# Optimization experiments

Hardware: AMD Instinct MI355X
Metric: run time of the kernel (lower is better)

The kernel has to match this reference:

```python
import jax, jax.numpy as jnp
import numpy as np

BN_EPS = 1e-5

def setup_inputs() -> dict:
    key = jax.random.key(0)
    ks = jax.random.split(key, 8)
    B, Cin, H, W = 4, 256, 64, 64
    Cqk, Cout = 128, 256
    x = jax.random.normal(ks[0], (B, Cin, H, W), dtype=jnp.float32)
    # 1x1 convs == per-pixel linear maps: weight [out, in], bias [out]
    Wq = jax.random.normal(ks[1], (Cqk, Cin), dtype=jnp.float32) * 0.05
    bq = jax.random.normal(ks[2], (Cqk,), dtype=jnp.float32) * 0.05
    Wk = jax.random.normal(ks[3], (Cqk, Cin), dtype=jnp.float32) * 0.05
    bk = jax.random.normal(ks[4], (Cqk,), dtype=jnp.float32) * 0.05
    Wv = jax.random.normal(ks[5], (Cout, Cin), dtype=jnp.float32) * 0.05
    bv = jax.random.normal(ks[6], (Cout,), dtype=jnp.float32) * 0.05
    gamma = jnp.ones((Cout,), dtype=jnp.float32)
    beta = jnp.zeros((Cout,), dtype=jnp.float32)
    return {"x": x, "Wq": Wq, "bq": bq, "Wk": Wk, "bk": bk,
            "Wv": Wv, "bv": bv, "gamma": gamma, "beta": beta}

def reference(x, Wq, bq, Wk, bk, Wv, bv, gamma, beta):
    B, Cin, H, W = x.shape
    N = H * W
    # 1x1 convs (per-pixel linear projections)
    q = jnp.einsum('bchw,oc->bohw', x, Wq) + bq[None, :, None, None]  # [B,Cqk,H,W]
    k = jnp.einsum('bchw,oc->bohw', x, Wk) + bk[None, :, None, None]  # [B,Cqk,H,W]
    v = jnp.einsum('bchw,oc->bohw', x, Wv) + bv[None, :, None, None]  # [B,Cout,H,W]
    # num_levels=1: bilinear interpolate to the same size is identity.
    qf = q.reshape(B, -1, N)   # [B,Cqk,N]
    kf = k.reshape(B, -1, N)   # [B,Cqk,N]
    vf = v.reshape(B, -1, N)   # [B,Cout,N]
    # score = q^T k, softmax over keys (no 1/sqrt(d) scaling, as in source)
    score = jnp.einsum('bcn,bcm->bnm', qf, kf)        # [B,N,N]
    att = jax.nn.softmax(score, axis=2)               # [B,N,N]
    w = jnp.einsum('bnm,bcm->bcn', att, vf)           # [B,Cout,N]
    merged = w.reshape(B, -1, H, W)                   # [B,Cout,H,W]
    # BatchNorm2d in training mode: batch stats over (B,H,W), biased variance
    mean = jnp.mean(merged, axis=(0, 2, 3), keepdims=True)
    var = jnp.var(merged, axis=(0, 2, 3), keepdims=True)
    norm = (merged - mean) * jax.lax.rsqrt(var + BN_EPS)
    return norm * gamma[None, :, None, None] + beta[None, :, None, None]
```

## Files before the change

### kernel.cpp

```cpp
#include <hip/hip_runtime.h>
#include <hip/hip_bf16.h>

typedef __attribute__((ext_vector_type(8))) _Float16 hfrag;
typedef __attribute__((ext_vector_type(4))) float ffrag;
typedef __attribute__((ext_vector_type(8))) unsigned short us8;
typedef __attribute__((ext_vector_type(4))) unsigned short us4;

#define DEVINL static __device__ __forceinline__
#define MFMAH(a, b, c)  __builtin_amdgcn_mfma_f32_16x16x32_f16((a), (b), (c), 0, 0, 0)

DEVINL void gload_lds16(const _Float16* g, _Float16* l) {
    __builtin_amdgcn_global_load_lds(
        (const __attribute__((address_space(1))) unsigned int*)g,
        (__attribute__((address_space(3))) unsigned int*)l, 16, 0, 0);
}

DEVINL int pkh(float a, float b) {
    typedef __attribute__((ext_vector_type(2))) __fp16 fp16x2;
    fp16x2 t = __builtin_amdgcn_cvt_pkrtz(a, b);
    union { fp16x2 h; int i; } u; u.h = t; return u.i;
}

DEVINL int permV(int p) {
    return (p & 35) | ((p & 8) << 1) | ((p & 4) << 1) | ((p & 16) >> 2);
}

__global__ void kprep(const float* __restrict__ Wq, const float* __restrict__ Wk,
                      const float* __restrict__ Wv, const float* __restrict__ bq,
                      const float* __restrict__ bk, const float* __restrict__ bv,
                      _Float16* __restrict__ Wh, float* __restrict__ ball) {
    int t = blockIdx.x * 256 + threadIdx.x;
    int o = t >> 8, c = t & 255;
    float v = (o < 128) ? Wq[o * 256 + c]
            : (o < 256) ? Wk[(o - 128) * 256 + c]
                        : Wv[(o - 256) * 256 + c];
    Wh[t] = (_Float16)v;
    if (c == 0) {
        ball[o] = (o < 128) ? bq[o] : (o < 256) ? bk[o - 128] : bv[o - 256];
    }
}

__global__ __launch_bounds__(256) void kproj(const float* __restrict__ x,
                                             const _Float16* __restrict__ Wh,
                                             const float* __restrict__ ball,
                                             _Float16* __restrict__ Qb,
                                             _Float16* __restrict__ Kb,
                                             _Float16* __restrict__ Vb) {
    __shared__ _Float16 sX[64 * 256];
    const int t = threadIdx.x;
    const int lane = t & 63;
    const int wv = t >> 6;
    const int l16 = lane & 15;
    const int lg = lane >> 4;
    const int b = blockIdx.x >> 6;
    const int n0 = (blockIdx.x & 63) << 6;
    const float* xb = x + (size_t)b * 256 * 4096 + n0;

    const int p = lane;
#pragma unroll
    for (int ci = 0; ci < 8; ++ci) {
        const int c0 = ci * 32 + (wv << 3);
        __align__(16) _Float16 th[8];
#pragma unroll
        for (int j = 0; j < 8; ++j) th[j] = (_Float16)xb[(size_t)(c0 + j) * 4096 + p];
        *(us8*)&sX[p * 256 + (c0 ^ ((p & 7) << 3))] = *(const us8*)th;
    }
    __syncthreads();

    ffrag accQK[16];
    ffrag accV[16];
#pragma unroll
    for (int i = 0; i < 16; ++i) {
        accQK[i] = ffrag{0.f, 0.f, 0.f, 0.f};
        accV[i]  = ffrag{0.f, 0.f, 0.f, 0.f};
    }
    const int rowx = 16 * wv + l16;
#pragma unroll
    for (int step = 0; step < 8; ++step) {
        const int cb = step * 32 + (lg << 3);
        hfrag ax = *(const hfrag*)&sX[rowx * 256 + (cb ^ ((rowx & 7) << 3))];
#pragma unroll
        for (int ct = 0; ct < 16; ++ct) {
            const int o = ct * 16 + l16;
            hfrag bw = *(const hfrag*)&Wh[o * 256 + cb];
            accQK[ct] = MFMAH(ax, bw, accQK[ct]);
        }
        hfrag bx[4];
#pragma unroll
        for (int c2 = 0; c2 < 4; ++c2) {
            const int px = c2 * 16 + l16;
            bx[c2] = *(const hfrag*)&sX[px * 256 + (cb ^ ((px & 7) << 3))];
        }
#pragma unroll
        for (int mt = 0; mt < 4; ++mt) {
            const int o = 256 + 64 * wv + 16 * mt + l16;
            hfrag aw = *(const hfrag*)&Wh[o * 256 + cb];
#pragma unroll
            for (int c2 = 0; c2 < 4; ++c2)
                accV[mt * 4 + c2] = MFMAH(aw, bx[c2], accV[mt * 4 + c2]);
        }
    }

#pragma unroll
    for (int ct = 0; ct < 16; ++ct) {
        const int o = ct * 16 + l16;
        const float bias = ball[o];
        _Float16* dst = (o < 128) ? Qb : Kb;
        const int oo = o & 127;
#pragma unroll
        for (int r = 0; r < 4; ++r) {
            const int px = 16 * wv + (lg << 2) + r;
            dst[((size_t)b * 4096 + n0 + px) * 128 + oo] = (_Float16)(accQK[ct][r] + bias);
        }
    }
#pragma unroll
    for (int mt = 0; mt < 4; ++mt) {
#pragma unroll
        for (int r = 0; r < 4; ++r) {
            const int o = 64 * wv + 16 * mt + (lg << 2) + r;
            const float bias = ball[256 + o];
#pragma unroll
            for (int c2 = 0; c2 < 4; ++c2) {
                const int px = c2 * 16 + l16;
                Vb[((size_t)b * 256 + o) * 4096 + n0 + permV(px)] =
                    (_Float16)(accV[mt * 4 + c2][r] + bias);
            }
        }
    }
}

__global__ __launch_bounds__(512, 4) void kattn(const _Float16* __restrict__ Qb,
                                                const _Float16* __restrict__ Kb,
                                                const _Float16* __restrict__ Vb,
                                                _Float16* __restrict__ pO,
                                                float* __restrict__ pML) {
    __shared__ __align__(16) _Float16 smem[24832];
    _Float16* sK = smem;
    _Float16* sV = smem + 8192;
    float* sml = (float*)(smem + 24576);

    const int t = threadIdx.x;
    const int lane = t & 63;
    const int wv = t >> 6;
    const int qg = wv & 3;
    const int kh = wv >> 2;
    const int l16 = lane & 15;
    const int lg = lane >> 4;

    const int blk = blockIdx.x;
    const int x8 = blk & 7;
    const int b = x8 >> 1;
    const int ksel = x8 & 1;
    const int qt4 = blk >> 3;
    const int n0 = qt4 << 6;
    const int kb = ksel << 11;

    const _Float16* Kg = Kb + (size_t)b * 4096 * 128;
    const _Float16* Vg = Vb + (size_t)b * 256 * 4096;

    hfrag aq[4];
    {
        const size_t gq = ((size_t)b * 4096 + n0 + 16 * qg + l16) * 128;
#pragma unroll
        for (int st = 0; st < 4; ++st)
            aq[st] = *(const hfrag*)&Qb[gq + st * 32 + lg * 8];
    }

    float m_ = -3e38f, l_ = 0.f;
    ffrag O[16];
#pragma unroll
    for (int i = 0; i < 16; ++i) O[i] = ffrag{0.f, 0.f, 0.f, 0.f};

    const int krow_in = lane >> 4;
    const int kcol = lane & 15;
    const int vrow_in = lane >> 3;
    const int vcol = lane & 7;

    for (int it = 0; it < 32; ++it) {
        const int k0 = kb + (it << 6);
        __builtin_amdgcn_s_barrier();
        __builtin_amdgcn_sched_barrier(0);
#pragma unroll
        for (int j = 0; j < 2; ++j) {
            const int c = 2 * wv + j;
            const int row = 4 * c + krow_in;
            gload_lds16(Kg + (size_t)(k0 + row) * 128 + ((kcol ^ (row & 7)) << 3),
                        sK + c * 512);
        }
        __builtin_amdgcn_sched_barrier(0);
#pragma unroll
        for (int j = 0; j < 4; ++j) {
            const int cv = 4 * wv + j;
            const int co = 8 * cv + vrow_in;
            gload_lds16(Vg + (size_t)co * 4096 + k0 + ((vcol ^ (co & 7)) << 3),
                        sV + cv * 512);
        }
        asm volatile("s_waitcnt vmcnt(4)" ::: "memory");
        __builtin_amdgcn_s_barrier();
        __builtin_amdgcn_sched_barrier(0);

        ffrag S[2];
        S[0] = ffrag{0.f, 0.f, 0.f, 0.f};
        S[1] = ffrag{0.f, 0.f, 0.f, 0.f};
#pragma unroll
        for (int kt = 0; kt < 2; ++kt) {
            const int rowk = kh * 32 + kt * 16 + l16;
            const int swz = (rowk & 7) << 3;
#pragma unroll
            for (int st = 0; st < 4; ++st) {
                hfrag ak = *(const hfrag*)&sK[rowk * 128 + ((st * 32 + lg * 8) ^ swz)];
                S[kt] = MFMAH(ak, aq[st], S[kt]);
            }
        }

        float mx = fmaxf(fmaxf(fmaxf(S[0][0], S[0][1]), fmaxf(S[0][2], S[0][3])),
                         fmaxf(fmaxf(S[1][0], S[1][1]), fmaxf(S[1][2], S[1][3])));
        mx = fmaxf(mx, __shfl_xor(mx, 16));
        mx = fmaxf(mx, __shfl_xor(mx, 32));
        if (__any(mx > m_ + 8.f)) {
            const float newm = fmaxf(m_, mx);
            const float sc = __expf(m_ - newm);
            m_ = newm;
            l_ *= sc;
#pragma unroll
            for (int i = 0; i < 16; ++i)
#pragma unroll
                for (int r = 0; r < 4; ++r) O[i][r] *= sc;
        }
        float e0[4], e1[4];
        float rs = 0.f;
#pragma unroll
        for (int r = 0; r < 4; ++r) {
            e0[r] = __expf(S[0][r] - m_);
            e1[r] = __expf(S[1][r] - m_);
            rs += e0[r] + e1[r];
        }
        rs += __shfl_xor(rs, 16);
        rs += __shfl_xor(rs, 32);
        l_ += rs;

        hfrag pb;
        {
            union { int i[4]; hfrag h; } u;
            u.i[0] = pkh(e0[0], e0[1]);
            u.i[1] = pkh(e0[2], e0[3]);
            u.i[2] = pkh(e1[0], e1[1]);
            u.i[3] = pkh(e1[2], e1[3]);
            pb = u.h;
        }

        asm volatile("s_waitcnt vmcnt(0)" ::: "memory");
        __builtin_amdgcn_s_barrier();
        __builtin_amdgcn_sched_barrier(0);

#pragma unroll
        for (int ct = 0; ct < 16; ++ct) {
            const int co = ct * 16 + l16;
            hfrag av = *(const hfrag*)&sV[co * 64 + ((kh * 32 + lg * 8) ^ ((co & 7) << 3))];
            O[ct] = MFMAH(av, pb, O[ct]);
        }
    }

    __syncthreads();
    _Float16* sE = smem;
    const int row = qg * 16 + l16;
    const int rsw = (row & 7) << 3;
    if (kh == 1) {
        const float invl = 1.f / l_;
#pragma unroll
        for (int ct = 0; ct < 16; ++ct)
#pragma unroll
            for (int r = 0; r < 4; ++r) {
                const int col = ct * 16 + lg * 4 + r;
                sE[row * 256 + (col ^ rsw)] = (_Float16)(O[ct][r] * invl);
            }
        if (lg == 0) ((float2*)sml)[row] = make_float2(m_, l_);
    }
    __syncthreads();
    const size_t mlbase = (size_t)(ksel * 4 + b) * 4096 + n0;
    if (kh == 0) {
        const float2 pml = ((const float2*)sml)[row];
        const float M = fmaxf(m_, pml.x);
        const float a = __expf(m_ - M), c = __expf(pml.x - M);
        const float newl = a * l_ + c * pml.y;
        const float wa = a / newl, wb = c * pml.y / newl;
        if (lg == 0) ((float2*)pML)[mlbase + row] = make_float2(M, newl);
#pragma unroll
        for (int ct = 0; ct < 16; ++ct)
#pragma unroll
            for (int r = 0; r < 4; ++r) {
                const int col = ct * 16 + lg * 4 + r;
                const int idx = row * 256 + (col ^ rsw);
                const float o1n = (float)sE[idx];
                sE[idx] = (_Float16)(wa * O[ct][r] + wb * o1n);
            }
    }
    __syncthreads();
    const size_t obase = ((size_t)(ksel * 4 + b) * 4096 + n0) * 256;
#pragma unroll
    for (int i = 0; i < 4; ++i) {
        const int idx = i * 512 + t;
        const int px = idx >> 5;
        const int cg = idx & 31;
        *(us8*)&pO[obase + (size_t)px * 256 + cg * 8] =
            *(const us8*)&sE[px * 256 + (cg ^ (px & 7)) * 8];
    }
}

__global__ __launch_bounds__(256) void kmerge(const _Float16* __restrict__ pO,
                                              const float* __restrict__ pML,
                                              _Float16* __restrict__ wbuf,
                                              float* __restrict__ part) {
    __shared__ float sacc[2048];
    __shared__ float sacc2[2048];
    const int t = threadIdx.x;
    const int rowloc = t >> 5;
    const int co8 = (t & 31) * 8;
    float s[8], s2[8];
#pragma unroll
    for (int j = 0; j < 8; ++j) { s[j] = 0.f; s2[j] = 0.f; }
#pragma unroll 2
    for (int i = 0; i < 8; ++i) {
        const int g = blockIdx.x * 64 + i * 8 + rowloc;
        const float2 ml0 = ((const float2*)pML)[g];
        const float2 ml1 = ((const float2*)pML)[16384 + g];
        const float M = fmaxf(ml0.x, ml1.x);
        const float a = __expf(ml0.x - M) * ml0.y;
        const float c = __expf(ml1.x - M) * ml1.y;
        const float inv = 1.f / (a + c);
        const float wa = a * inv, wc = c * inv;
        hfrag o0 = *(const hfrag*)&pO[(size_t)g * 256 + co8];
        hfrag o1 = *(const hfrag*)&pO[(size_t)(16384 + g) * 256 + co8];
        hfrag w;
#pragma unroll
        for (int j = 0; j < 8; ++j) {
            const float v = wa * (float)o0[j] + wc * (float)o1[j];
            w[j] = (_Float16)v;
            s[j] += v;
            s2[j] += v * v;
        }
        *(hfrag*)&wbuf[(size_t)g * 256 + co8] = w;
    }
#pragma unroll
    for (int j = 0; j < 8; ++j) {
        sacc[rowloc * 256 + co8 + j] = s[j];
        sacc2[rowloc * 256 + co8 + j] = s2[j];
    }
    __syncthreads();
    float p = 0.f, p2 = 0.f;
#pragma unroll
    for (int rl = 0; rl < 8; ++rl) {
        p  += sacc[rl * 256 + t];
        p2 += sacc2[rl * 256 + t];
    }
    part[blockIdx.x * 512 + t] = p;
    part[blockIdx.x * 512 + 256 + t] = p2;
}

__global__ void kstats2(const float* __restrict__ partial, float* __restrict__ stats) {
    const int ch = blockIdx.x;
    const int j = threadIdx.x;
    float s = 0.f;
#pragma unroll
    for (int i = 0; i < 4; ++i)
        s += partial[(size_t)(j + 64 * i) * 512 + ch];
    s += __shfl_xor(s, 1);
    s += __shfl_xor(s, 2);
    s += __shfl_xor(s, 4);
    s += __shfl_xor(s, 8);
    s += __shfl_xor(s, 16);
    s += __shfl_xor(s, 32);
    if (j == 0) stats[ch] = s;
}

__global__ __launch_bounds__(256) void kapply(const _Float16* __restrict__ w,
                                              const float* __restrict__ stats,
                                              const float* __restrict__ gamma,
                                              const float* __restrict__ beta,
                                              float* __restrict__ out) {
    __shared__ _Float16 sw[64 * 260];
    __shared__ float sscale[256];
    __shared__ float sshift[256];
    const int t = threadIdx.x;
    const int b = blockIdx.x >> 6;
    const int n0 = (blockIdx.x & 63) << 6;
    const _Float16* wb = w + ((size_t)b * 4096 + n0) * 256;
#pragma unroll
    for (int i = 0; i < 16; ++i) {
        const int chunk = i * 256 + t;
        const int p = chunk >> 6;
        const int cq = chunk & 63;
        *(us4*)&sw[p * 260 + cq * 4] = *(const us4*)&wb[p * 256 + cq * 4];
    }
    {
        const float mean = stats[t] * (1.f / 16384.f);
        const float var = stats[256 + t] * (1.f / 16384.f) - mean * mean;
        const float inv = rsqrtf(var + 1e-5f);
        const float sc = gamma[t] * inv;
        sscale[t] = sc;
        sshift[t] = beta[t] - mean * sc;
    }
    __syncthreads();
    const int p = t & 63;
    const int cg = t >> 6;
    float* ob = out + (size_t)b * 256 * 4096 + n0;
#pragma unroll 4
    for (int i = 0; i < 64; ++i) {
        const int co = i * 4 + cg;
        const float v = (float)sw[p * 260 + co];
        ob[(size_t)co * 4096 + p] = v * sscale[co] + sshift[co];
    }
}

extern "C" void kernel_launch(void* const* d_in, const int* in_sizes, int n_in,
                              void* d_out, int out_size, void* d_ws, size_t ws_size,
                              hipStream_t stream) {
    const float* x     = (const float*)d_in[0];
    const float* Wq    = (const float*)d_in[1];
    const float* bq    = (const float*)d_in[2];
    const float* Wk    = (const float*)d_in[3];
    const float* bk    = (const float*)d_in[4];
    const float* Wv    = (const float*)d_in[5];
    const float* bv    = (const float*)d_in[6];
    const float* gamma = (const float*)d_in[7];
    const float* beta  = (const float*)d_in[8];
    float* out = (float*)d_out;

    char* ws = (char*)d_ws;
    _Float16* Wh    = (_Float16*)(ws + 0x0);
    float*    pML   = (float*)(ws + 0x0);
    float*    ball  = (float*)(ws + 0x40000);
    float*    stats = (float*)(ws + 0x40800);
    float*    part  = (float*)(ws + 0x41000);
    _Float16* Qb    = (_Float16*)(ws + 0x100000);
    _Float16* Kb    = (_Float16*)(ws + 0x500000);
    _Float16* wbuf  = (_Float16*)(ws + 0x100000);
    _Float16* Vb    = (_Float16*)(ws + 0x900000);
    _Float16* pO    = (_Float16*)(ws + 0x1100000);
    if (ws_size < 0x2100000) return;

    kprep<<<512, 256, 0, stream>>>(Wq, Wk, Wv, bq, bk, bv, Wh, ball);
    kproj<<<256, 256, 0, stream>>>(x, Wh, ball, Qb, Kb, Vb);
    kattn<<<512, 512, 0, stream>>>(Qb, Kb, Vb, pO, pML);
    kmerge<<<256, 256, 0, stream>>>(pO, pML, wbuf, part);
    kstats2<<<512, 64, 0, stream>>>(part, stats);
    kapply<<<256, 256, 0, stream>>>(wbuf, stats, gamma, beta, out);
}
```

Before: 143.9 us.

## Have each attention wave process two query tiles to reuse K/V fragments

```diff
diff --git a/kernel.cpp b/kernel.cpp
--- a/kernel.cpp
+++ b/kernel.cpp
@@ -129,7 +129,7 @@
     }
 }
 
-__global__ __launch_bounds__(512, 4) void kattn(const _Float16* __restrict__ Qb,
+__global__ __launch_bounds__(256, 2) void kattn(const _Float16* __restrict__ Qb,
                                                 const _Float16* __restrict__ Kb,
                                                 const _Float16* __restrict__ Vb,
                                                 _Float16* __restrict__ pO,
@@ -142,8 +142,8 @@
     const int t = threadIdx.x;
     const int lane = t & 63;
     const int wv = t >> 6;
-    const int qg = wv & 3;
-    const int kh = wv >> 2;
+    const int qg = wv & 1;
+    const int kh = wv >> 1;
     const int l16 = lane & 15;
     const int lg = lane >> 4;
 
@@ -158,18 +158,25 @@
     const _Float16* Kg = Kb + (size_t)b * 4096 * 128;
     const _Float16* Vg = Vb + (size_t)b * 256 * 4096;
 
-    hfrag aq[4];
+    hfrag aq0[4], aq1[4];
     {
-        const size_t gq = ((size_t)b * 4096 + n0 + 16 * qg + l16) * 128;
-#pragma unroll
-        for (int st = 0; st < 4; ++st)
-            aq[st] = *(const hfrag*)&Qb[gq + st * 32 + lg * 8];
-    }
-
-    float m_ = -3e38f, l_ = 0.f;
-    ffrag O[16];
-#pragma unroll
-    for (int i = 0; i < 16; ++i) O[i] = ffrag{0.f, 0.f, 0.f, 0.f};
+        const size_t gq0 = ((size_t)b * 4096 + n0 + qg * 32 + l16) * 128;
+        const size_t gq1 = gq0 + 16 * 128;
+#pragma unroll
+        for (int st = 0; st < 4; ++st) {
+            aq0[st] = *(const hfrag*)&Qb[gq0 + st * 32 + lg * 8];
+            aq1[st] = *(const hfrag*)&Qb[gq1 + st * 32 + lg * 8];
+        }
+    }
+
+    float m0 = -3e38f, l0 = 0.f;
+    float m1 = -3e38f, l1 = 0.f;
+    ffrag O0[16], O1[16];
+#pragma unroll
+    for (int i = 0; i < 16; ++i) {
+        O0[i] = ffrag{0.f, 0.f, 0.f, 0.f};
+        O1[i] = ffrag{0.f, 0.f, 0.f, 0.f};
+    }
 
     const int krow_in = lane >> 4;
     const int kcol = lane & 15;
@@ -181,27 +188,26 @@
         __builtin_amdgcn_s_barrier();
         __builtin_amdgcn_sched_barrier(0);
 #pragma unroll
-        for (int j = 0; j < 2; ++j) {
-            const int c = 2 * wv + j;
+        for (int j = 0; j < 4; ++j) {
+            const int c = 4 * wv + j;
             const int row = 4 * c + krow_in;
             gload_lds16(Kg + (size_t)(k0 + row) * 128 + ((kcol ^ (row & 7)) << 3),
                         sK + c * 512);
         }
         __builtin_amdgcn_sched_barrier(0);
 #pragma unroll
-        for (int j = 0; j < 4; ++j) {
-            const int cv = 4 * wv + j;
+        for (int j = 0; j < 8; ++j) {
+            const int cv = 8 * wv + j;
             const int co = 8 * cv + vrow_in;
             gload_lds16(Vg + (size_t)co * 4096 + k0 + ((vcol ^ (co & 7)) << 3),
                         sV + cv * 512);
         }
-        asm volatile("s_waitcnt vmcnt(4)" ::: "memory");
+        asm volatile("s_waitcnt vmcnt(8)" ::: "memory");
         __builtin_amdgcn_s_barrier();
         __builtin_amdgcn_sched_barrier(0);
 
-        ffrag S[2];
-        S[0] = ffrag{0.f, 0.f, 0.f, 0.f};
-        S[1] = ffrag{0.f, 0.f, 0.f, 0.f};
+        ffrag S00 = ffrag{0.f,0.f,0.f,0.f}, S01 = ffrag{0.f,0.f,0.f,0.f};
+        ffrag S10 = ffrag{0.f,0.f,0.f,0.f}, S11 = ffrag{0.f,0.f,0.f,0.f};
 #pragma unroll
         for (int kt = 0; kt < 2; ++kt) {
             const int rowk = kh * 32 + kt * 16 + l16;
@@ -209,44 +215,69 @@
 #pragma unroll
             for (int st = 0; st < 4; ++st) {
                 hfrag ak = *(const hfrag*)&sK[rowk * 128 + ((st * 32 + lg * 8) ^ swz)];
-                S[kt] = MFMAH(ak, aq[st], S[kt]);
+                if (kt == 0) {
+                    S00 = MFMAH(ak, aq0[st], S00);
+                    S10 = MFMAH(ak, aq1[st], S10);
+                } else {
+                    S01 = MFMAH(ak, aq0[st], S01);
+                    S11 = MFMAH(ak, aq1[st], S11);
+                }
             }
         }
 
-        float mx = fmaxf(fmaxf(fmaxf(S[0][0], S[0][1]), fmaxf(S[0][2], S[0][3])),
-                         fmaxf(fmaxf(S[1][0], S[1][1]), fmaxf(S[1][2], S[1][3])));
-        mx = fmaxf(mx, __shfl_xor(mx, 16));
-        mx = fmaxf(mx, __shfl_xor(mx, 32));
-        if (__any(mx > m_ + 8.f)) {
-            const float newm = fmaxf(m_, mx);
-            const float sc = __expf(m_ - newm);
-            m_ = newm;
-            l_ *= sc;
-#pragma unroll
-            for (int i = 0; i < 16; ++i)
-#pragma unroll
-                for (int r = 0; r < 4; ++r) O[i][r] *= sc;
-        }
-        float e0[4], e1[4];
-        float rs = 0.f;
+        float mx0 = fmaxf(fmaxf(fmaxf(S00[0], S00[1]), fmaxf(S00[2], S00[3])),
+                          fmaxf(fmaxf(S01[0], S01[1]), fmaxf(S01[2], S01[3])));
+        float mx1 = fmaxf(fmaxf(fmaxf(S10[0], S10[1]), fmaxf(S10[2], S10[3])),
+                          fmaxf(fmaxf(S11[0], S11[1]), fmaxf(S11[2], S11[3])));
+        mx0 = fmaxf(mx0, __shfl_xor(mx0, 16));
+        mx0 = fmaxf(mx0, __shfl_xor(mx0, 32));
+        mx1 = fmaxf(mx1, __shfl_xor(mx1, 16));
+        mx1 = fmaxf(mx1, __shfl_xor(mx1, 32));
+        if (__any((mx0 > m0 + 8.f) || (mx1 > m1 + 8.f))) {
+            const float nm0 = fmaxf(m0, mx0), nm1 = fmaxf(m1, mx1);
+            const float sc0 = __expf(m0 - nm0), sc1 = __expf(m1 - nm1);
+            m0 = nm0; m1 = nm1;
+            l0 *= sc0; l1 *= sc1;
+#pragma unroll
+            for (int i = 0; i < 16; ++i) {
+#pragma unroll
+                for (int r = 0; r < 4; ++r) {
+                    O0[i][r] *= sc0;
+                    O1[i][r] *= sc1;
+                }
+            }
+        }
+        float e00[4], e01[4], e10[4], e11[4];
+        float rs0 = 0.f, rs1 = 0.f;
 #pragma unroll
         for (int r = 0; r < 4; ++r) {
-            e0[r] = __expf(S[0][r] - m_);
-            e1[r] = __expf(S[1][r] - m_);
-            rs += e0[r] + e1[r];
-        }
-        rs += __shfl_xor(rs, 16);
-        rs += __shfl_xor(rs, 32);
-        l_ += rs;
-
-        hfrag pb;
+            e00[r] = __expf(S00[r] - m0);
+            e01[r] = __expf(S01[r] - m0);
+            e10[r] = __expf(S10[r] - m1);
+            e11[r] = __expf(S11[r] - m1);
+            rs0 += e00[r] + e01[r];
+            rs1 += e10[r] + e11[r];
+        }
+        rs0 += __shfl_xor(rs0, 16);
+        rs0 += __shfl_xor(rs0, 32);
+        rs1 += __shfl_xor(rs1, 16);
+        rs1 += __shfl_xor(rs1, 32);
+        l0 += rs0;
+        l1 += rs1;
+
+        hfrag pb0, pb1;
         {
             union { int i[4]; hfrag h; } u;
-            u.i[0] = pkh(e0[0], e0[1]);
-            u.i[1] = pkh(e0[2], e0[3]);
-            u.i[2] = pkh(e1[0], e1[1]);
-            u.i[3] = pkh(e1[2], e1[3]);
-            pb = u.h;
+            u.i[0] = pkh(e00[0], e00[1]);
+            u.i[1] = pkh(e00[2], e00[3]);
+            u.i[2] = pkh(e01[0], e01[1]);
+            u.i[3] = pkh(e01[2], e01[3]);
+            pb0 = u.h;
+            u.i[0] = pkh(e10[0], e10[1]);
+            u.i[1] = pkh(e10[2], e10[3]);
+            u.i[2] = pkh(e11[0], e11[1]);
+            u.i[3] = pkh(e11[2], e11[3]);
+            pb1 = u.h;
         }
 
         asm volatile("s_waitcnt vmcnt(0)" ::: "memory");
@@ -257,49 +288,66 @@
         for (int ct = 0; ct < 16; ++ct) {
             const int co = ct * 16 + l16;
             hfrag av = *(const hfrag*)&sV[co * 64 + ((kh * 32 + lg * 8) ^ ((co & 7) << 3))];
-            O[ct] = MFMAH(av, pb, O[ct]);
+            O0[ct] = MFMAH(av, pb0, O0[ct]);
+            O1[ct] = MFMAH(av, pb1, O1[ct]);
         }
     }
 
     __syncthreads();
     _Float16* sE = smem;
-    const int row = qg * 16 + l16;
-    const int rsw = (row & 7) << 3;
+    const int r0 = qg * 32 + l16;
+    const int r1 = r0 + 16;
+    const int rsw0 = (r0 & 7) << 3;
+    const int rsw1 = (r1 & 7) << 3;
     if (kh == 1) {
-        const float invl = 1.f / l_;
+        const float inv0 = 1.f / l0, inv1 = 1.f / l1;
 #pragma unroll
         for (int ct = 0; ct < 16; ++ct)
 #pragma unroll
             for (int r = 0; r < 4; ++r) {
                 const int col = ct * 16 + lg * 4 + r;
-                sE[row * 256 + (col ^ rsw)] = (_Float16)(O[ct][r] * invl);
+                sE[r0 * 256 + (col ^ rsw0)] = (_Float16)(O0[ct][r] * inv0);
+                sE[r1 * 256 + (col ^ rsw1)] = (_Float16)(O1[ct][r] * inv1);
             }
-        if (lg == 0) ((float2*)sml)[row] = make_float2(m_, l_);
+        if (lg == 0) {
+            ((float2*)sml)[r0] = make_float2(m0, l0);
+            ((float2*)sml)[r1] = make_float2(m1, l1);
+        }
     }
     __syncthreads();
     const size_t mlbase = (size_t)(ksel * 4 + b) * 4096 + n0;
     if (kh == 0) {
-        const float2 pml = ((const float2*)sml)[row];
-        const float M = fmaxf(m_, pml.x);
-        const float a = __expf(m_ - M), c = __expf(pml.x - M);
-        const float newl = a * l_ + c * pml.y;
-        const float wa = a / newl, wb = c * pml.y / newl;
-        if (lg == 0) ((float2*)pML)[mlbase + row] = make_float2(M, newl);
+        const float2 pml0 = ((const float2*)sml)[r0];
+        const float2 pml1 = ((const float2*)sml)[r1];
+        const float M0 = fmaxf(m0, pml0.x), M1 = fmaxf(m1, pml1.x);
+        const float a0 = __expf(m0 - M0), c0 = __expf(pml0.x - M0);
+        const float a1 = __expf(m1 - M1), c1 = __expf(pml1.x - M1);
+        const float nl0 = a0 * l0 + c0 * pml0.y;
+        const float nl1 = a1 * l1 + c1 * pml1.y;
+        const float wa0 = a0 / nl0, wb0 = c0 * pml0.y / nl0;
+        const float wa1 = a1 / nl1, wb1 = c1 * pml1.y / nl1;
+        if (lg == 0) {
+            ((float2*)pML)[mlbase + r0] = make_float2(M0, nl0);
+            ((float2*)pML)[mlbase + r1] = make_float2(M1, nl1);
+        }
 #pragma unroll
         for (int ct = 0; ct < 16; ++ct)
 #pragma unroll
             for (int r = 0; r < 4; ++r) {
                 const int col = ct * 16 + lg * 4 + r;
-                const int idx = row * 256 + (col ^ rsw);
-                const float o1n = (float)sE[idx];
-                sE[idx] = (_Float16)(wa * O[ct][r] + wb * o1n);
+                const int i0 = r0 * 256 + (col ^ rsw0);
+                const int i1 = r1 * 256 + (col ^ rsw1);
+                const float v0 = (float)sE[i0];
+                const float v1 = (float)sE[i1];
+                sE[i0] = (_Float16)(wa0 * O0[ct][r] + wb0 * v0);
+                sE[i1] = (_Float16)(wa1 * O1[ct][r] + wb1 * v1);
             }
     }
     __syncthreads();
     const size_t obase = ((size_t)(ksel * 4 + b) * 4096 + n0) * 256;
 #pragma unroll
-    for (int i = 0; i < 4; ++i) {
-        const int idx = i * 512 + t;
+    for (int i = 0; i < 8; ++i) {
+        const int idx = i * 256 + t;
         const int px = idx >> 5;
         const int cg = idx & 31;
         *(us8*)&pO[obase + (size_t)px * 256 + cg * 8] =
@@ -441,7 +489,7 @@
 
     kprep<<<512, 256, 0, stream>>>(Wq, Wk, Wv, bq, bk, bv, Wh, ball);
     kproj<<<256, 256, 0, stream>>>(x, Wh, ball, Qb, Kb, Vb);
-    kattn<<<512, 512, 0, stream>>>(Qb, Kb, Vb, pO, pML);
+    kattn<<<512, 256, 0, stream>>>(Qb, Kb, Vb, pO, pML);
     kmerge<<<256, 256, 0, stream>>>(pO, pML, wbuf, part);
     kstats2<<<512, 64, 0, stream>>>(part, stats);
     kapply<<<256, 256, 0, stream>>>(wbuf, stats, gamma, beta, out);
```

Result: no change. 144.9 us (+0.7%).
